# Performance work log

Measured on AMD Instinct MI355X. Metric: run time of the kernel, lower is better.

## Reference

```python
import jax, jax.numpy as jnp
import numpy as np

N_HIDDEN_LAYERS = 9  # 32->32 middle layers (plus input 1->32 and output 32->1)
HID = 32
SLOPE = 0.01  # LeakyReLU negative_slope


def leaky_relu(x):
    return jnp.where(x >= 0, x, SLOPE * x)


def setup_inputs() -> dict:
    key = jax.random.key(0)
    ks = jax.random.split(key, 8)
    N = 1048576
    x = jax.random.normal(ks[0], (N,), dtype=jnp.float32)
    # PyTorch Linear init: U(-1/sqrt(fan_in), 1/sqrt(fan_in))
    def u(k, shape, fan_in):
        b = 1.0 / np.sqrt(fan_in)
        return jax.random.uniform(k, shape, jnp.float32, -b, b)
    W_in = u(ks[1], (1, HID), 1)
    b_in = u(ks[2], (HID,), 1)
    W_hid = u(ks[3], (N_HIDDEN_LAYERS, HID, HID), HID)
    b_hid = u(ks[4], (N_HIDDEN_LAYERS, HID), HID)
    W_out = u(ks[5], (HID, 1), HID)
    b_out = u(ks[6], (1,), HID)
    return {"x": x, "W_in": W_in, "b_in": b_in, "W_hid": W_hid,
            "b_hid": b_hid, "W_out": W_out, "b_out": b_out}


def reference(x, W_in, b_in, W_hid, b_hid, W_out, b_out):
    N = x.shape[0]
    h = x[:, None]  # [N, 1], mirrors x.reshape(N, 1)
    h = leaky_relu(h @ W_in + b_in)  # [N, 32]
    def step(h, wb):
        W, b = wb
        return leaky_relu(h @ W + b), None
    h, _ = jax.lax.scan(step, h, (W_hid, b_hid))
    out = h @ W_out + b_out  # [N, 1]
    return out.reshape(1, N)
```

## Files before the change

kernel.cpp:

```cpp
#include <hip/hip_runtime.h>

#define NLAYERS 9
#define HID 32
#define SLOPE 0.01f

typedef _Float16 v2h __attribute__((ext_vector_type(2)));
typedef _Float16 v8h __attribute__((ext_vector_type(8)));
typedef float v4f __attribute__((ext_vector_type(4)));

#define NCHAIN 4

union U8 { v8h v; v2h p[4]; };

__device__ __forceinline__ v2h pk_cvt(float a, float b) {
    return __builtin_bit_cast(v2h, __builtin_amdgcn_cvt_pkrtz(a, b));
}
__device__ __forceinline__ v2h leaky2(v2h t, v2h s) {
    return __builtin_elementwise_max(t, t * s);
}
__device__ __forceinline__ int umap(int g, int j) {
    return 4 * g + (j & 3) + 16 * (j >> 2);
}

__global__ __launch_bounds__(256, 3) void mlp_mfma_kernel(
    const float* __restrict__ x,
    const float* __restrict__ W_in,
    const float* __restrict__ b_in,
    const float* __restrict__ W_hid,
    const float* __restrict__ b_hid,
    const float* __restrict__ W_out,
    const float* __restrict__ b_out,
    float* __restrict__ out, int N)
{
    __shared__ __align__(16) _Float16 wA_sh[NLAYERS][2][64][8];
    __shared__ __align__(64) float bc_sh[NLAYERS][2][16];

    const int tid = threadIdx.x;
    for (int t = tid; t < NLAYERS * 2 * 64; t += blockDim.x) {
        int l = t >> 7, r = t & 127, tt = (r >> 6) & 1, ln = r & 63;
        int i = ln & 15, g = ln >> 4;
        const float* Wl = W_hid + l * HID * HID;
        v8h w;
#pragma unroll
        for (int j = 0; j < 8; ++j)
            w[j] = (_Float16)Wl[umap(g, j) * HID + 16 * tt + i];
        *(v8h*)&wA_sh[l][tt][ln][0] = w;
    }
    for (int t = tid; t < NLAYERS * HID; t += blockDim.x)
        ((float*)bc_sh)[t] = b_hid[t];
    __syncthreads();

    const int lane = tid & 63;
    const int g    = lane >> 4;
    const int col  = lane & 15;

    v2h win2[4], bin2[4], wout2[4];
#pragma unroll
    for (int jj = 0; jj < 4; ++jj) {
        int u0 = umap(g, 2 * jj), u1 = umap(g, 2 * jj + 1);
        win2[jj]  = v2h{(_Float16)W_in[u0],  (_Float16)W_in[u1]};
        bin2[jj]  = v2h{(_Float16)b_in[u0],  (_Float16)b_in[u1]};
        wout2[jj] = v2h{(_Float16)W_out[u0], (_Float16)W_out[u1]};
    }
    const float bo = b_out[0];
    const v2h slope2 = v2h{(_Float16)SLOPE, (_Float16)SLOPE};

    const int nwaves = (gridDim.x * blockDim.x) >> 6;
    const int wid    = (blockIdx.x * blockDim.x + tid) >> 6;
    const int niter  = (N + NCHAIN * 32 - 1) / (NCHAIN * 32);

    float xc[2 * NCHAIN] = {};
    if (wid < niter) {
#pragma unroll
        for (int c = 0; c < NCHAIN; ++c)
#pragma unroll
            for (int nh = 0; nh < 2; ++nh) {
                int idx = wid * (NCHAIN * 32) + c * 32 + 16 * nh + col;
                xc[2 * c + nh] = (idx < N) ? x[idx] : 0.0f;
            }
    }

    for (int it = wid; it < niter; it += nwaves) {
        float xn[2 * NCHAIN] = {};
        {
            int nit = it + nwaves;
            if (nit < niter) {
#pragma unroll
                for (int c = 0; c < NCHAIN; ++c)
#pragma unroll
                    for (int nh = 0; nh < 2; ++nh) {
                        int idx = nit * (NCHAIN * 32) + c * 32 + 16 * nh + col;
                        xn[2 * c + nh] = (idx < N) ? x[idx] : 0.0f;
                    }
            }
        }

        U8 f[NCHAIN][2];
#pragma unroll
        for (int c = 0; c < NCHAIN; ++c)
#pragma unroll
            for (int nh = 0; nh < 2; ++nh) {
                _Float16 xh = (_Float16)xc[2 * c + nh];
                v2h x2 = v2h{xh, xh};
#pragma unroll
                for (int jj = 0; jj < 4; ++jj)
                    f[c][nh].p[jj] = leaky2(x2 * win2[jj] + bin2[jj], slope2);
            }

        v8h wA0 = *(const v8h*)&wA_sh[0][0][lane][0];
        v8h wA1 = *(const v8h*)&wA_sh[0][1][lane][0];
        v4f bc0 = *(const v4f*)&bc_sh[0][0][4 * g];
        v4f bc1 = *(const v4f*)&bc_sh[0][1][4 * g];
#pragma unroll 1
        for (int l = 0; l < NLAYERS; ++l) {
            const int lnx = (l + 1 < NLAYERS) ? l + 1 : l;
            v8h wA0n = *(const v8h*)&wA_sh[lnx][0][lane][0];
            v8h wA1n = *(const v8h*)&wA_sh[lnx][1][lane][0];
            v4f bc0n = *(const v4f*)&bc_sh[lnx][0][4 * g];
            v4f bc1n = *(const v4f*)&bc_sh[lnx][1][4 * g];
#pragma unroll
            for (int gr = 0; gr < NCHAIN / 2; ++gr) {
                const int c0 = 2 * gr, c1 = 2 * gr + 1;
                v4f a0t0h0 = __builtin_amdgcn_mfma_f32_16x16x32_f16(wA0, f[c0][0].v, bc0, 0, 0, 0);
                v4f a0t0h1 = __builtin_amdgcn_mfma_f32_16x16x32_f16(wA0, f[c0][1].v, bc0, 0, 0, 0);
                v4f a0t1h0 = __builtin_amdgcn_mfma_f32_16x16x32_f16(wA1, f[c0][0].v, bc1, 0, 0, 0);
                v4f a0t1h1 = __builtin_amdgcn_mfma_f32_16x16x32_f16(wA1, f[c0][1].v, bc1, 0, 0, 0);
                v4f a1t0h0 = __builtin_amdgcn_mfma_f32_16x16x32_f16(wA0, f[c1][0].v, bc0, 0, 0, 0);
                v4f a1t0h1 = __builtin_amdgcn_mfma_f32_16x16x32_f16(wA0, f[c1][1].v, bc0, 0, 0, 0);
                v4f a1t1h0 = __builtin_amdgcn_mfma_f32_16x16x32_f16(wA1, f[c1][0].v, bc1, 0, 0, 0);
                v4f a1t1h1 = __builtin_amdgcn_mfma_f32_16x16x32_f16(wA1, f[c1][1].v, bc1, 0, 0, 0);
                f[c0][0].p[0] = leaky2(pk_cvt(a0t0h0[0], a0t0h0[1]), slope2);
                f[c0][0].p[1] = leaky2(pk_cvt(a0t0h0[2], a0t0h0[3]), slope2);
                f[c0][0].p[2] = leaky2(pk_cvt(a0t1h0[0], a0t1h0[1]), slope2);
                f[c0][0].p[3] = leaky2(pk_cvt(a0t1h0[2], a0t1h0[3]), slope2);
                f[c0][1].p[0] = leaky2(pk_cvt(a0t0h1[0], a0t0h1[1]), slope2);
                f[c0][1].p[1] = leaky2(pk_cvt(a0t0h1[2], a0t0h1[3]), slope2);
                f[c0][1].p[2] = leaky2(pk_cvt(a0t1h1[0], a0t1h1[1]), slope2);
                f[c0][1].p[3] = leaky2(pk_cvt(a0t1h1[2], a0t1h1[3]), slope2);
                f[c1][0].p[0] = leaky2(pk_cvt(a1t0h0[0], a1t0h0[1]), slope2);
                f[c1][0].p[1] = leaky2(pk_cvt(a1t0h0[2], a1t0h0[3]), slope2);
                f[c1][0].p[2] = leaky2(pk_cvt(a1t1h0[0], a1t1h0[1]), slope2);
                f[c1][0].p[3] = leaky2(pk_cvt(a1t1h0[2], a1t1h0[3]), slope2);
                f[c1][1].p[0] = leaky2(pk_cvt(a1t0h1[0], a1t0h1[1]), slope2);
                f[c1][1].p[1] = leaky2(pk_cvt(a1t0h1[2], a1t0h1[3]), slope2);
                f[c1][1].p[2] = leaky2(pk_cvt(a1t1h1[0], a1t1h1[1]), slope2);
                f[c1][1].p[3] = leaky2(pk_cvt(a1t1h1[2], a1t1h1[3]), slope2);
            }
            wA0 = wA0n; wA1 = wA1n; bc0 = bc0n; bc1 = bc1n;
        }

#pragma unroll
        for (int c = 0; c < NCHAIN; ++c)
#pragma unroll
            for (int nh = 0; nh < 2; ++nh) {
                float p = 0.0f;
#pragma unroll
                for (int jj = 0; jj < 4; ++jj)
                    p = __builtin_amdgcn_fdot2(f[c][nh].p[jj], wout2[jj], p, false);
                p += __shfl_xor(p, 16, 64);
                p += __shfl_xor(p, 32, 64);
                float o = p + bo;
                int idx = it * (NCHAIN * 32) + c * 32 + 16 * nh + col;
                if (g == 2 * (c & 1) + nh && idx < N) out[idx] = o;
            }

#pragma unroll
        for (int q = 0; q < 2 * NCHAIN; ++q) xc[q] = xn[q];
    }
}

extern "C" void kernel_launch(void* const* d_in, const int* in_sizes, int n_in,
                              void* d_out, int out_size, void* d_ws, size_t ws_size,
                              hipStream_t stream) {
    const float* x     = (const float*)d_in[0];
    const float* W_in  = (const float*)d_in[1];
    const float* b_in  = (const float*)d_in[2];
    const float* W_hid = (const float*)d_in[3];
    const float* b_hid = (const float*)d_in[4];
    const float* W_out = (const float*)d_in[5];
    const float* b_out = (const float*)d_in[6];
    float* out = (float*)d_out;

    int N = in_sizes[0];
    dim3 block(256);
    dim3 grid(768);
    mlp_mfma_kernel<<<grid, block, 0, stream>>>(x, W_in, b_in, W_hid, b_hid,
                                                W_out, b_out, out, N);
}
```

Baseline: 92.67 us.

## Raise chains per wave to six with software-pipelined MFMA/activation interleave

Each wave now processes six 32-sample chains per iteration instead of four. Within each layer the MFMAs for one chain group are issued while the LeakyReLU/convert work of the previous group runs, so MFMA latency is hidden by independent work. Prefetched inputs are stored as packed fp16 pairs to save registers, and occupancy is reduced (launch bounds 2, grid 512) to fit the larger register footprint. The trade-off is fewer resident waves available to hide latency, plus a tail imbalance because N is not a multiple of 192.

```diff
diff --git a/kernel.cpp b/kernel.cpp
--- a/kernel.cpp
+++ b/kernel.cpp
@@ -8,7 +8,7 @@
 typedef _Float16 v8h __attribute__((ext_vector_type(8)));
 typedef float v4f __attribute__((ext_vector_type(4)));
 
-#define NCHAIN 4
+#define NCHAIN 6
 
 union U8 { v8h v; v2h p[4]; };
 
@@ -22,7 +22,7 @@
     return 4 * g + (j & 3) + 16 * (j >> 2);
 }
 
-__global__ __launch_bounds__(256, 3) void mlp_mfma_kernel(
+__global__ __launch_bounds__(256, 2) void mlp_mfma_kernel(
     const float* __restrict__ x,
     const float* __restrict__ W_in,
     const float* __restrict__ b_in,
@@ -38,12 +38,12 @@
     const int tid = threadIdx.x;
     for (int t = tid; t < NLAYERS * 2 * 64; t += blockDim.x) {
         int l = t >> 7, r = t & 127, tt = (r >> 6) & 1, ln = r & 63;
-        int i = ln & 15, g = ln >> 4;
+        int i = ln & 15, gg = ln >> 4;
         const float* Wl = W_hid + l * HID * HID;
         v8h w;
 #pragma unroll
         for (int j = 0; j < 8; ++j)
-            w[j] = (_Float16)Wl[umap(g, j) * HID + 16 * tt + i];
+            w[j] = (_Float16)Wl[umap(gg, j) * HID + 16 * tt + i];
         *(v8h*)&wA_sh[l][tt][ln][0] = w;
     }
     for (int t = tid; t < NLAYERS * HID; t += blockDim.x)
@@ -69,29 +69,35 @@
     const int wid    = (blockIdx.x * blockDim.x + tid) >> 6;
     const int niter  = (N + NCHAIN * 32 - 1) / (NCHAIN * 32);
 
-    float xc[2 * NCHAIN] = {};
+    v2h xc2[NCHAIN];
+#pragma unroll
+    for (int c = 0; c < NCHAIN; ++c) xc2[c] = v2h{(_Float16)0.f, (_Float16)0.f};
     if (wid < niter) {
 #pragma unroll
-        for (int c = 0; c < NCHAIN; ++c)
-#pragma unroll
-            for (int nh = 0; nh < 2; ++nh) {
-                int idx = wid * (NCHAIN * 32) + c * 32 + 16 * nh + col;
-                xc[2 * c + nh] = (idx < N) ? x[idx] : 0.0f;
-            }
+        for (int c = 0; c < NCHAIN; ++c) {
+            int i0 = wid * (NCHAIN * 32) + c * 32 + col;
+            int i1 = i0 + 16;
+            float a = (i0 < N) ? x[i0] : 0.0f;
+            float b = (i1 < N) ? x[i1] : 0.0f;
+            xc2[c] = pk_cvt(a, b);
+        }
     }
 
     for (int it = wid; it < niter; it += nwaves) {
-        float xn[2 * NCHAIN] = {};
+        v2h xn2[NCHAIN];
+#pragma unroll
+        for (int c = 0; c < NCHAIN; ++c) xn2[c] = v2h{(_Float16)0.f, (_Float16)0.f};
         {
             int nit = it + nwaves;
             if (nit < niter) {
 #pragma unroll
-                for (int c = 0; c < NCHAIN; ++c)
-#pragma unroll
-                    for (int nh = 0; nh < 2; ++nh) {
-                        int idx = nit * (NCHAIN * 32) + c * 32 + 16 * nh + col;
-                        xn[2 * c + nh] = (idx < N) ? x[idx] : 0.0f;
-                    }
+                for (int c = 0; c < NCHAIN; ++c) {
+                    int i0 = nit * (NCHAIN * 32) + c * 32 + col;
+                    int i1 = i0 + 16;
+                    float a = (i0 < N) ? x[i0] : 0.0f;
+                    float b = (i1 < N) ? x[i1] : 0.0f;
+                    xn2[c] = pk_cvt(a, b);
+                }
             }
         }
 
@@ -100,7 +106,7 @@
         for (int c = 0; c < NCHAIN; ++c)
 #pragma unroll
             for (int nh = 0; nh < 2; ++nh) {
-                _Float16 xh = (_Float16)xc[2 * c + nh];
+                _Float16 xh = xc2[c][nh];
                 v2h x2 = v2h{xh, xh};
 #pragma unroll
                 for (int jj = 0; jj < 4; ++jj)
@@ -118,34 +124,63 @@
             v8h wA1n = *(const v8h*)&wA_sh[lnx][1][lane][0];
             v4f bc0n = *(const v4f*)&bc_sh[lnx][0][4 * g];
             v4f bc1n = *(const v4f*)&bc_sh[lnx][1][4 * g];
-#pragma unroll
-            for (int gr = 0; gr < NCHAIN / 2; ++gr) {
-                const int c0 = 2 * gr, c1 = 2 * gr + 1;
-                v4f a0t0h0 = __builtin_amdgcn_mfma_f32_16x16x32_f16(wA0, f[c0][0].v, bc0, 0, 0, 0);
-                v4f a0t0h1 = __builtin_amdgcn_mfma_f32_16x16x32_f16(wA0, f[c0][1].v, bc0, 0, 0, 0);
-                v4f a0t1h0 = __builtin_amdgcn_mfma_f32_16x16x32_f16(wA1, f[c0][0].v, bc1, 0, 0, 0);
-                v4f a0t1h1 = __builtin_amdgcn_mfma_f32_16x16x32_f16(wA1, f[c0][1].v, bc1, 0, 0, 0);
-                v4f a1t0h0 = __builtin_amdgcn_mfma_f32_16x16x32_f16(wA0, f[c1][0].v, bc0, 0, 0, 0);
-                v4f a1t0h1 = __builtin_amdgcn_mfma_f32_16x16x32_f16(wA0, f[c1][1].v, bc0, 0, 0, 0);
-                v4f a1t1h0 = __builtin_amdgcn_mfma_f32_16x16x32_f16(wA1, f[c1][0].v, bc1, 0, 0, 0);
-                v4f a1t1h1 = __builtin_amdgcn_mfma_f32_16x16x32_f16(wA1, f[c1][1].v, bc1, 0, 0, 0);
-                f[c0][0].p[0] = leaky2(pk_cvt(a0t0h0[0], a0t0h0[1]), slope2);
-                f[c0][0].p[1] = leaky2(pk_cvt(a0t0h0[2], a0t0h0[3]), slope2);
-                f[c0][0].p[2] = leaky2(pk_cvt(a0t1h0[0], a0t1h0[1]), slope2);
-                f[c0][0].p[3] = leaky2(pk_cvt(a0t1h0[2], a0t1h0[3]), slope2);
-                f[c0][1].p[0] = leaky2(pk_cvt(a0t0h1[0], a0t0h1[1]), slope2);
-                f[c0][1].p[1] = leaky2(pk_cvt(a0t0h1[2], a0t0h1[3]), slope2);
-                f[c0][1].p[2] = leaky2(pk_cvt(a0t1h1[0], a0t1h1[1]), slope2);
-                f[c0][1].p[3] = leaky2(pk_cvt(a0t1h1[2], a0t1h1[3]), slope2);
-                f[c1][0].p[0] = leaky2(pk_cvt(a1t0h0[0], a1t0h0[1]), slope2);
-                f[c1][0].p[1] = leaky2(pk_cvt(a1t0h0[2], a1t0h0[3]), slope2);
-                f[c1][0].p[2] = leaky2(pk_cvt(a1t1h0[0], a1t1h0[1]), slope2);
-                f[c1][0].p[3] = leaky2(pk_cvt(a1t1h0[2], a1t1h0[3]), slope2);
-                f[c1][1].p[0] = leaky2(pk_cvt(a1t0h1[0], a1t0h1[1]), slope2);
-                f[c1][1].p[1] = leaky2(pk_cvt(a1t0h1[2], a1t0h1[3]), slope2);
-                f[c1][1].p[2] = leaky2(pk_cvt(a1t1h1[0], a1t1h1[1]), slope2);
-                f[c1][1].p[3] = leaky2(pk_cvt(a1t1h1[2], a1t1h1[3]), slope2);
-            }
+
+            v4f A0[2][4], A1[2][4], A2[2][4];
+#pragma unroll
+            for (int q = 0; q < 2; ++q) {
+                A0[q][0] = __builtin_amdgcn_mfma_f32_16x16x32_f16(wA0, f[q][0].v, bc0, 0, 0, 0);
+                A0[q][1] = __builtin_amdgcn_mfma_f32_16x16x32_f16(wA0, f[q][1].v, bc0, 0, 0, 0);
+                A0[q][2] = __builtin_amdgcn_mfma_f32_16x16x32_f16(wA1, f[q][0].v, bc1, 0, 0, 0);
+                A0[q][3] = __builtin_amdgcn_mfma_f32_16x16x32_f16(wA1, f[q][1].v, bc1, 0, 0, 0);
+            }
+#pragma unroll
+            for (int q = 0; q < 2; ++q) {
+                A1[q][0] = __builtin_amdgcn_mfma_f32_16x16x32_f16(wA0, f[2 + q][0].v, bc0, 0, 0, 0);
+                A1[q][1] = __builtin_amdgcn_mfma_f32_16x16x32_f16(wA0, f[2 + q][1].v, bc0, 0, 0, 0);
+                A1[q][2] = __builtin_amdgcn_mfma_f32_16x16x32_f16(wA1, f[2 + q][0].v, bc1, 0, 0, 0);
+                A1[q][3] = __builtin_amdgcn_mfma_f32_16x16x32_f16(wA1, f[2 + q][1].v, bc1, 0, 0, 0);
+            }
+#pragma unroll
+            for (int q = 0; q < 2; ++q) {
+                f[q][0].p[0] = leaky2(pk_cvt(A0[q][0][0], A0[q][0][1]), slope2);
+                f[q][0].p[1] = leaky2(pk_cvt(A0[q][0][2], A0[q][0][3]), slope2);
+                f[q][0].p[2] = leaky2(pk_cvt(A0[q][2][0], A0[q][2][1]), slope2);
+                f[q][0].p[3] = leaky2(pk_cvt(A0[q][2][2], A0[q][2][3]), slope2);
+                f[q][1].p[0] = leaky2(pk_cvt(A0[q][1][0], A0[q][1][1]), slope2);
+                f[q][1].p[1] = leaky2(pk_cvt(A0[q][1][2], A0[q][1][3]), slope2);
+                f[q][1].p[2] = leaky2(pk_cvt(A0[q][3][0], A0[q][3][1]), slope2);
+                f[q][1].p[3] = leaky2(pk_cvt(A0[q][3][2], A0[q][3][3]), slope2);
+            }
+#pragma unroll
+            for (int q = 0; q < 2; ++q) {
+                A2[q][0] = __builtin_amdgcn_mfma_f32_16x16x32_f16(wA0, f[4 + q][0].v, bc0, 0, 0, 0);
+                A2[q][1] = __builtin_amdgcn_mfma_f32_16x16x32_f16(wA0, f[4 + q][1].v, bc0, 0, 0, 0);
+                A2[q][2] = __builtin_amdgcn_mfma_f32_16x16x32_f16(wA1, f[4 + q][0].v, bc1, 0, 0, 0);
+                A2[q][3] = __builtin_amdgcn_mfma_f32_16x16x32_f16(wA1, f[4 + q][1].v, bc1, 0, 0, 0);
+            }
+#pragma unroll
+            for (int q = 0; q < 2; ++q) {
+                f[2 + q][0].p[0] = leaky2(pk_cvt(A1[q][0][0], A1[q][0][1]), slope2);
+                f[2 + q][0].p[1] = leaky2(pk_cvt(A1[q][0][2], A1[q][0][3]), slope2);
+                f[2 + q][0].p[2] = leaky2(pk_cvt(A1[q][2][0], A1[q][2][1]), slope2);
+                f[2 + q][0].p[3] = leaky2(pk_cvt(A1[q][2][2], A1[q][2][3]), slope2);
+                f[2 + q][1].p[0] = leaky2(pk_cvt(A1[q][1][0], A1[q][1][1]), slope2);
+                f[2 + q][1].p[1] = leaky2(pk_cvt(A1[q][1][2], A1[q][1][3]), slope2);
+                f[2 + q][1].p[2] = leaky2(pk_cvt(A1[q][3][0], A1[q][3][1]), slope2);
+                f[2 + q][1].p[3] = leaky2(pk_cvt(A1[q][3][2], A1[q][3][3]), slope2);
+            }
+#pragma unroll
+            for (int q = 0; q < 2; ++q) {
+                f[4 + q][0].p[0] = leaky2(pk_cvt(A2[q][0][0], A2[q][0][1]), slope2);
+                f[4 + q][0].p[1] = leaky2(pk_cvt(A2[q][0][2], A2[q][0][3]), slope2);
+                f[4 + q][0].p[2] = leaky2(pk_cvt(A2[q][2][0], A2[q][2][1]), slope2);
+                f[4 + q][0].p[3] = leaky2(pk_cvt(A2[q][2][2], A2[q][2][3]), slope2);
+                f[4 + q][1].p[0] = leaky2(pk_cvt(A2[q][1][0], A2[q][1][1]), slope2);
+                f[4 + q][1].p[1] = leaky2(pk_cvt(A2[q][1][2], A2[q][1][3]), slope2);
+                f[4 + q][1].p[2] = leaky2(pk_cvt(A2[q][3][0], A2[q][3][1]), slope2);
+                f[4 + q][1].p[3] = leaky2(pk_cvt(A2[q][3][2], A2[q][3][3]), slope2);
+            }
+
             wA0 = wA0n; wA1 = wA1n; bc0 = bc0n; bc1 = bc1n;
         }
 
@@ -161,11 +196,11 @@
                 p += __shfl_xor(p, 32, 64);
                 float o = p + bo;
                 int idx = it * (NCHAIN * 32) + c * 32 + 16 * nh + col;
-                if (g == 2 * (c & 1) + nh && idx < N) out[idx] = o;
-            }
-
-#pragma unroll
-        for (int q = 0; q < 2 * NCHAIN; ++q) xc[q] = xn[q];
+                if (((2 * c + nh) & 3) == g && idx < N) out[idx] = o;
+            }
+
+#pragma unroll
+        for (int c = 0; c < NCHAIN; ++c) xc2[c] = xn2[c];
     }
 }
 
@@ -183,7 +218,7 @@
 
     int N = in_sizes[0];
     dim3 block(256);
-    dim3 grid(768);
+    dim3 grid(512);
     mlp_mfma_kernel<<<grid, block, 0, stream>>>(x, W_in, b_in, W_hid, b_hid,
                                                 W_out, b_out, out, N);
 }
```

Measured after the change: 97.21 us. +4.9%, slower.
